# Performance work log

Measured on AMD Instinct MI355X. Metric: run time of the kernel, lower is better.

The kernel has to match this reference:

```python
import jax, jax.numpy as jnp
import numpy as np

T, B, S, L = 256, 128, 256, 2
H, E, V = 512, 512, 32000


def setup_inputs() -> dict:
    key = jax.random.key(0)
    ks = jax.random.split(key, 17)
    n = lambda k, shape, s=0.05: jax.random.normal(k, shape, dtype=jnp.float32) * s
    tokens = jax.random.randint(ks[0], (T, B), 0, V)
    emb = n(ks[1], (V, E)).at[0].set(0.0)  # padding_idx=0 row zeroed
    return {
        "tokens": tokens,
        "h0": n(ks[2], (L, B, H)),
        "c0": n(ks[3], (L, B, H)),
        "context": n(ks[4], (S, B, H)),
        "init_output": n(ks[5], (B, H)),
        "emb": emb,
        "W_ih0": n(ks[6], (4 * H, E + H)),
        "b_ih0": n(ks[7], (4 * H,)),
        "W_hh0": n(ks[8], (4 * H, H)),
        "b_hh0": n(ks[9], (4 * H,)),
        "W_ih1": n(ks[10], (4 * H, H)),
        "b_ih1": n(ks[11], (4 * H,)),
        "W_hh1": n(ks[12], (4 * H, H)),
        "b_hh1": n(ks[13], (4 * H,)),
        "W_in": n(ks[14], (H, H)),
        "W_out": n(ks[15], (H, 2 * H)),
    }


def _lstm_cell(x, h, c, Wi, bi, Wh, bh):
    # torch LSTMCell: gates ordered i, f, g, o
    g = x @ Wi.T + bi + h @ Wh.T + bh
    i, f, gg, o = jnp.split(g, 4, axis=-1)
    c2 = jax.nn.sigmoid(f) * c + jax.nn.sigmoid(i) * jnp.tanh(gg)
    h2 = jax.nn.sigmoid(o) * jnp.tanh(c2)
    return h2, c2


def reference(tokens, h0, c0, context, init_output, emb,
              W_ih0, b_ih0, W_hh0, b_hh0, W_ih1, b_ih1, W_hh1, b_hh1,
              W_in, W_out):
    emb_seq = emb[tokens]                      # [T, B, E]
    ctx = jnp.transpose(context, (1, 0, 2))    # [B, S, H] (context.transpose(0,1))

    def step(carry, e_t):
        h, c, out = carry                      # h,c: [L,B,H]; out: [B,H]
        x = jnp.concatenate([e_t, out], axis=1)  # input feed
        h0_, c0_ = _lstm_cell(x, h[0], c[0], W_ih0, b_ih0, W_hh0, b_hh0)
        h1_, c1_ = _lstm_cell(h0_, h[1], c[1], W_ih1, b_ih1, W_hh1, b_hh1)
        rnn_out = h1_                          # dropout is identity at p=0 / eval
        # GlobalAttention (Luong general): score = ctx @ (W_in h)
        q = rnn_out @ W_in.T                   # [B, H]
        scores = jnp.einsum('bsh,bh->bs', ctx, q)
        a = jax.nn.softmax(scores, axis=-1)    # [B, S]
        wc = jnp.einsum('bs,bsh->bh', a, ctx)  # weighted context
        attn_out = jnp.tanh(jnp.concatenate([wc, rnn_out], axis=1) @ W_out.T)
        new_h = jnp.stack([h0_, h1_])
        new_c = jnp.stack([c0_, c1_])
        return (new_h, new_c, attn_out), (attn_out, a)

    (hF, cF, _), (outputs, attns) = jax.lax.scan(step, (h0, c0, init_output), emb_seq)
    return outputs, hF, cF, attns[-1]
```

## Files before the change

kernel.cpp:

```cpp
#include <hip/hip_runtime.h>
#include <hip/hip_bf16.h>
#include <math.h>

#define TT 256
#define BB 128
#define SS 256
#define HH 512
#define EE 512
#define NBLK 128
#define NTHR 512
#define BH (BB * HH)

typedef __attribute__((ext_vector_type(4))) float f32x4;
typedef __attribute__((ext_vector_type(8))) short s16x8;
typedef unsigned long long u64;

__device__ __forceinline__ float b2f(short v) {
    union { unsigned u; float f; } c;
    c.u = ((unsigned)(unsigned short)v) << 16;
    return c.f;
}
__device__ __forceinline__ short f2b(float f) {
    union { float f; unsigned u; } c; c.f = f;
    unsigned u = c.u;
    unsigned r = (u + 0x7fffu + ((u >> 16) & 1u)) >> 16;
    return (short)r;
}
__device__ __forceinline__ float sigm(float x) { return 1.f / (1.f + __expf(-x)); }

__device__ __forceinline__ u64 aldq(const void* p) {
    return __hip_atomic_load((const u64*)p, __ATOMIC_RELAXED, __HIP_MEMORY_SCOPE_AGENT);
}
__device__ __forceinline__ void ast2(short* p, short v) {
    __hip_atomic_store(p, v, __ATOMIC_RELAXED, __HIP_MEMORY_SCOPE_AGENT);
}
__device__ __forceinline__ s16x8 ald16(const void* p) {
    s16x8 r;
    asm volatile("global_load_dwordx4 %0, %1, off sc0 sc1" : "=v"(r) : "v"(p) : "memory");
    return r;
}

__device__ __forceinline__ void lbar() {
    asm volatile("s_waitcnt lgkmcnt(0)" ::: "memory");
    __builtin_amdgcn_s_barrier();
}


__global__ void k_pack2(const float* __restrict__ Wa, int ka, const float* __restrict__ Wb, int kb,
                        short* __restrict__ dst, int n) {
    const int K = ka + kb;
    for (int i = blockIdx.x * blockDim.x + threadIdx.x; i < n; i += gridDim.x * blockDim.x) {
        int g = i / K, k = i - g * K;
        float v = (k < ka) ? Wa[(size_t)g * ka + k] : Wb[(size_t)g * kb + (k - ka)];
        dst[i] = f2b(v);
    }
}

__global__ void k_bias(const float* __restrict__ a, const float* __restrict__ b, float* __restrict__ o,
                       const float* __restrict__ a2, const float* __restrict__ b2, float* __restrict__ o2) {
    int i = blockIdx.x * blockDim.x + threadIdx.x;
    if (i < 2048) { o[i] = a[i] + b[i]; o2[i] = a2[i] + b2[i]; }
}

__global__ void k_emb(const int* __restrict__ tok, const float* __restrict__ emb, short* __restrict__ Ebf) {
    const int n = TT * BB * EE;
    for (int i = blockIdx.x * blockDim.x + threadIdx.x; i < n; i += gridDim.x * blockDim.x) {
        int tb = i >> 9, k = i & 511;
        int t = tok[tb];
        Ebf[i] = f2b(emb[(size_t)t * EE + k]);
    }
}

__global__ __launch_bounds__(512) void k_cvt8(const float* __restrict__ ctx, const short* __restrict__ Wb,
                                              int wstride, int transpose, unsigned char* __restrict__ out8) {
    const int tid = threadIdx.x, w = tid >> 6, l = tid & 63;
    const int m0 = blockIdx.y * 128, n0 = blockIdx.x * 64;
    const int kc8 = (l >> 4) * 8;
    const int m = m0 + w * 16 + (l & 15);
    const int b = m >> 8, s = m & 255;
    const float* arow = ctx + ((size_t)s * BB + b) * HH + kc8;
    f32x4 acc[4];
    const f32x4 zero = {0.f, 0.f, 0.f, 0.f};
#pragma unroll
    for (int j = 0; j < 4; ++j) acc[j] = zero;
#pragma unroll
    for (int kc = 0; kc < 16; ++kc) {
        const int k0 = kc * 32;
        float4 x0 = *reinterpret_cast<const float4*>(arow + k0);
        float4 x1 = *reinterpret_cast<const float4*>(arow + k0 + 4);
        s16x8 afr;
        afr[0] = f2b(x0.x); afr[1] = f2b(x0.y); afr[2] = f2b(x0.z); afr[3] = f2b(x0.w);
        afr[4] = f2b(x1.x); afr[5] = f2b(x1.y); afr[6] = f2b(x1.z); afr[7] = f2b(x1.w);
#pragma unroll
        for (int j = 0; j < 4; ++j) {
            s16x8 bfr = *reinterpret_cast<const s16x8*>(Wb + (size_t)(n0 + j * 16 + (l & 15)) * wstride + k0 + kc8);
            acc[j] = __builtin_amdgcn_mfma_f32_16x16x32_bf16(afr, bfr, acc[j], 0, 0, 0);
        }
    }
#pragma unroll
    for (int j = 0; j < 4; ++j)
#pragma unroll
        for (int r = 0; r < 4; ++r) {
            const int mm = m0 + w * 16 + (l >> 4) * 4 + r;
            const int nn = n0 + j * 16 + (l & 15);
            unsigned char v8 = (unsigned char)(__builtin_amdgcn_cvt_pk_fp8_f32(acc[j][r], 0.f, 0, false) & 0xff);
            if (transpose) {
                const int bb = mm >> 8, ss = mm & 255;
                out8[((size_t)bb * HH + nn) * SS + ss] = v8;
            } else {
                out8[(size_t)mm * HH + nn] = v8;
            }
        }
}

__global__ void k_state(const float* __restrict__ h0in, const float* __restrict__ iout,
                        short* __restrict__ h0x, short* __restrict__ h1x, short* __restrict__ outx) {
    int i = blockIdx.x * blockDim.x + threadIdx.x;
    if (i < BH) {
        h0x[i] = f2b(h0in[i]);
        h1x[i] = f2b(h0in[BH + i]);
        outx[i] = f2b(iout[i]);
    }
}


struct P {
    const short* Ebf;
    const float* c0in;
    const unsigned char* ctxW8;
    const unsigned char* ctxO8T;
    const short* Woutb;
    const short* W0cat;
    const short* W1cat;
    const float* bias0;
    const float* bias1;
    short* h0x;
    short* h1x;
    short* outx;
    float* dout;
    unsigned* flags;
};

#define MFMA16(a, b, c) __builtin_amdgcn_mfma_f32_16x16x32_bf16((a), (b), (c), 0, 0, 0)
#define MFMA8(a, b, c) __builtin_amdgcn_mfma_f32_16x16x32_fp8_fp8((a), (b), (c), 0, 0, 0)

__device__ __forceinline__ s16x8 ldsfrag(const short* base, int stride, int row, int col8) {
    return *reinterpret_cast<const s16x8*>(base + row * stride + ((col8 ^ (row & 7)) << 3));
}

__device__ __forceinline__ void issue8(const short* __restrict__ src, int tid, int khalf, s16x8* q) {
#pragma unroll
    for (int c = 0; c < 8; ++c) {
        const int chunk = c * 512 + tid;
        const int row = chunk >> 5, col8 = chunk & 31;
        q[c] = ald16(src + row * HH + khalf * 256 + col8 * 8);
    }
}
template <int N>
__device__ __forceinline__ void write8n(short* __restrict__ stg, int tid, const s16x8* q) {
    asm volatile("s_waitcnt vmcnt(%0)" ::"i"(N) : "memory");
#pragma unroll
    for (int c = 0; c < 8; ++c) {
        const int chunk = c * 512 + tid;
        const int row = chunk >> 5, col8 = chunk & 31;
        *reinterpret_cast<s16x8*>(stg + row * 256 + ((col8 ^ (row & 7)) << 3)) = q[c];
    }
}

__device__ __forceinline__ f32x4 seg8(const short* stgp, const short* Ws, int wstride, int wbase,
                                      int mrow, int wrow, int kq, f32x4 acc) {
#pragma unroll
    for (int seg = 0; seg < 8; ++seg)
        acc = MFMA16(ldsfrag(stgp, 256, mrow, seg * 4 + kq),
                     ldsfrag(Ws, wstride, wrow, wbase + seg * 4 + kq), acc);
    return acc;
}

__device__ __forceinline__ void gbar(unsigned* flags, unsigned target) {
    asm volatile("s_waitcnt vmcnt(0)" ::: "memory");
    __syncthreads();
    if (threadIdx.x == 0)
        __hip_atomic_store(&flags[blockIdx.x * 16], target, __ATOMIC_RELAXED, __HIP_MEMORY_SCOPE_AGENT);
    if (threadIdx.x < NBLK) {
        while (__hip_atomic_load(&flags[threadIdx.x * 16], __ATOMIC_RELAXED, __HIP_MEMORY_SCOPE_AGENT) < target)
            __builtin_amdgcn_s_sleep(8);
    }
    __syncthreads();
}

__global__ void __launch_bounds__(NTHR, 1) coop_k(P p) {
    extern __shared__ __align__(16) char smem[];
    short* W0s = (short*)smem;
    short* W1s = W0s + 16 * 1536;
    short* stg = W1s + 16 * 1024;
    float* smallf = (float*)(stg + 128 * 256);
    float* bias0s = smallf;
    float* bias1s = smallf + 16;
    float* red = smallf + 32;
    float* scv = smallf + 48;
    float* aU = smallf + 304;
    short* h1b = (short*)(smallf + 560);
    unsigned* h18u = (unsigned*)(smallf + 816);
    unsigned* a32 = (unsigned*)(smallf + 944);

    const int tid = threadIdx.x;
    const int blk = blockIdx.x;
    const int l = tid & 63;
    const int w = tid >> 6;
    const int lrow = l & 15;
    const int mrow = w * 16 + lrow;
    const int kq = l >> 4;
    const size_t OFF_HF = (size_t)TT * BH;
    const size_t OFF_CF = OFF_HF + 2 * (size_t)BH;
    const size_t OFF_AT = OFF_CF + 2 * (size_t)BH;
    const f32x4 fz = {0.f, 0.f, 0.f, 0.f};

    for (int idx = tid; idx < 16 * 192; idx += NTHR) {
        int row = idx / 192, col8 = idx % 192;
        int g = (row & 3) * 512 + blk * 4 + (row >> 2);
        *reinterpret_cast<s16x8*>(W0s + row * 1536 + ((col8 ^ (row & 7)) << 3)) =
            *reinterpret_cast<const s16x8*>(p.W0cat + (size_t)g * 1536 + col8 * 8);
    }
    for (int idx = tid; idx < 16 * 128; idx += NTHR) {
        int row = idx / 128, col8 = idx % 128;
        int g = (row & 3) * 512 + blk * 4 + (row >> 2);
        *reinterpret_cast<s16x8*>(W1s + row * 1024 + ((col8 ^ (row & 7)) << 3)) =
            *reinterpret_cast<const s16x8*>(p.W1cat + (size_t)g * 1024 + col8 * 8);
    }
    if (tid < 16) {
        int g = (tid & 3) * 512 + blk * 4 + (tid >> 2);
        bias0s[tid] = p.bias0[g];
        bias1s[tid] = p.bias1[g];
    }
    __syncthreads();

    const int bA = tid >> 2;
    const int jA = blk * 4 + (tid & 3);
    float c0reg = p.c0in[bA * HH + jA];
    float c1reg = p.c0in[BH + bA * HH + jA];
    unsigned ep = 0;
    s16x8 qa[8], qb[8], qc[8], qd[8];

    for (int t = 0; t < TT; ++t) {
        const size_t pB = (size_t)(t & 1) * BH;
        const size_t pN = (size_t)((t & 1) ^ 1) * BH;

        {
            issue8(p.outx + pB, tid, 0, qa);
            issue8(p.outx + pB, tid, 1, qb);
            f32x4 aE = fz, aO = fz, aH = fz;
            {
                const short* erow = p.Ebf + ((size_t)t * BB + mrow) * EE + kq * 8;
#pragma unroll
                for (int seg = 0; seg < 16; ++seg) {
                    s16x8 afr = *reinterpret_cast<const s16x8*>(erow + seg * 32);
                    aE = MFMA16(afr, ldsfrag(W0s, 1536, lrow, seg * 4 + kq), aE);
                }
            }
            write8n<8>(stg, tid, qa);
            issue8(p.h0x + pB, tid, 0, qc);
            lbar();
            aO = seg8(stg, W0s, 1536, 64, mrow, lrow, kq, aO);
            lbar();
            write8n<8>(stg, tid, qb);
            issue8(p.h0x + pB, tid, 1, qd);
            lbar();
            aO = seg8(stg, W0s, 1536, 96, mrow, lrow, kq, aO);
            lbar();
            write8n<8>(stg, tid, qc);
            lbar();
            aH = seg8(stg, W0s, 1536, 128, mrow, lrow, kq, aH);
            lbar();
            write8n<0>(stg, tid, qd);
            lbar();
            aH = seg8(stg, W0s, 1536, 160, mrow, lrow, kq, aH);

            f32x4 acc = aE + aO + aH;
            lbar();
            float* scr = (float*)stg + w * 272;
#pragma unroll
            for (int r = 0; r < 4; ++r) scr[lrow * 17 + kq * 4 + r] = acc[r];
            const int bloc = l >> 2;
            const int n0 = (l & 3) * 4;
            float gi = scr[(n0 + 0) * 17 + bloc] + bias0s[n0 + 0];
            float gf = scr[(n0 + 1) * 17 + bloc] + bias0s[n0 + 1];
            float gg = scr[(n0 + 2) * 17 + bloc] + bias0s[n0 + 2];
            float go = scr[(n0 + 3) * 17 + bloc] + bias0s[n0 + 3];
            float cn = sigm(gf) * c0reg + sigm(gi) * tanhf(gg);
            float hn = sigm(go) * tanhf(cn);
            c0reg = cn;
            ast2(&p.h0x[pN + bA * HH + jA], f2b(hn));
            if (t == TT - 1) {
                p.dout[OFF_HF + bA * HH + jA] = hn;
                p.dout[OFF_CF + bA * HH + jA] = cn;
            }
        }
        gbar(p.flags, ++ep);

        {
            issue8(p.h0x + pN, tid, 0, qa);
            issue8(p.h0x + pN, tid, 1, qb);
            f32x4 b0 = fz, b1 = fz;
            write8n<8>(stg, tid, qa);
            issue8(p.h1x + pB, tid, 0, qc);
            lbar();
            b0 = seg8(stg, W1s, 1024, 0, mrow, lrow, kq, b0);
            lbar();
            write8n<8>(stg, tid, qb);
            issue8(p.h1x + pB, tid, 1, qd);
            lbar();
            b0 = seg8(stg, W1s, 1024, 32, mrow, lrow, kq, b0);
            lbar();
            write8n<8>(stg, tid, qc);
            lbar();
            b1 = seg8(stg, W1s, 1024, 64, mrow, lrow, kq, b1);
            lbar();
            write8n<0>(stg, tid, qd);
            lbar();
            b1 = seg8(stg, W1s, 1024, 96, mrow, lrow, kq, b1);

            f32x4 acc = b0 + b1;
            lbar();
            float* scr = (float*)stg + w * 272;
#pragma unroll
            for (int r = 0; r < 4; ++r) scr[lrow * 17 + kq * 4 + r] = acc[r];
            const int bloc = l >> 2;
            const int n0 = (l & 3) * 4;
            float gi = scr[(n0 + 0) * 17 + bloc] + bias1s[n0 + 0];
            float gf = scr[(n0 + 1) * 17 + bloc] + bias1s[n0 + 1];
            float gg = scr[(n0 + 2) * 17 + bloc] + bias1s[n0 + 2];
            float go = scr[(n0 + 3) * 17 + bloc] + bias1s[n0 + 3];
            float cn = sigm(gf) * c1reg + sigm(gi) * tanhf(gg);
            float hn = sigm(go) * tanhf(cn);
            c1reg = cn;
            ast2(&p.h1x[pN + bA * HH + jA], f2b(hn));
            if (t == TT - 1) {
                p.dout[OFF_HF + BH + bA * HH + jA] = hn;
                p.dout[OFF_CF + BH + bA * HH + jA] = cn;
            }
        }
        gbar(p.flags, ++ep);

        {
            float* pFh = (float*)stg;
            if (tid < 128) {
                union { u64 v; short s[4]; } c;
                c.v = aldq(p.h1x + pN + blk * HH + tid * 4);
#pragma unroll
                for (int j = 0; j < 4; ++j) h1b[tid * 4 + j] = c.s[j];
                float f0 = b2f(c.s[0]), f1 = b2f(c.s[1]), f2 = b2f(c.s[2]), f3 = b2f(c.s[3]);
                unsigned lo = __builtin_amdgcn_cvt_pk_fp8_f32(f0, f1, 0, false) & 0xffffu;
                unsigned hi = __builtin_amdgcn_cvt_pk_fp8_f32(f2, f3, 0, false) & 0xffffu;
                h18u[tid] = lo | (hi << 16);
            }
            lbar();
            {
                const unsigned char* cwb = p.ctxW8 + (size_t)blk * SS * HH;
                const u64* h18q = (const u64*)h18u;
#pragma unroll
                for (int i = 0; i < 2; ++i) {
                    const int s0 = (w * 2 + i) * 16;
                    f32x4 acc = fz;
#pragma unroll
                    for (int kc = 0; kc < 16; ++kc) {
                        const int k0 = kc * 32;
                        long long av = (long long)h18q[(k0 >> 3) + kq];
                        long long bv = *reinterpret_cast<const long long*>(cwb + (size_t)(s0 + lrow) * HH + k0 + kq * 8);
                        acc = MFMA8(av, bv, acc);
                    }
                    if (l < 16) scv[s0 + l] = acc[0];
                }
            }
            lbar();
            float sc = -1e30f, e = 0.f;
            if (tid < 256) sc = scv[tid];
            float mx = sc;
#pragma unroll
            for (int off = 32; off; off >>= 1) mx = fmaxf(mx, __shfl_xor(mx, off));
            if (l == 0 && tid < 256) red[w] = mx;
            lbar();
            const float M = fmaxf(fmaxf(red[0], red[1]), fmaxf(red[2], red[3]));
            if (tid < 256) { e = __expf(sc - M); aU[tid] = e; }
            float se = e;
#pragma unroll
            for (int off = 32; off; off >>= 1) se += __shfl_xor(se, off);
            if (l == 0 && tid < 256) red[8 + w] = se;
            lbar();
            const float inv = 1.f / (red[8] + red[9] + red[10] + red[11]);
            if (t == TT - 1 && tid < 256) p.dout[OFF_AT + blk * SS + tid] = aU[tid] * inv;
            if (tid < 64) {
                unsigned lo = __builtin_amdgcn_cvt_pk_fp8_f32(aU[tid * 4], aU[tid * 4 + 1], 0, false) & 0xffffu;
                unsigned hi = __builtin_amdgcn_cvt_pk_fp8_f32(aU[tid * 4 + 2], aU[tid * 4 + 3], 0, false) & 0xffffu;
                a32[tid] = lo | (hi << 16);
            }
            f32x4 gacc[4];
#pragma unroll
            for (int i = 0; i < 4; ++i) {
                const int j0 = (w * 4 + i) * 16;
                f32x4 acc = fz;
#pragma unroll
                for (int kc = 0; kc < 16; ++kc) {
                    const int k0 = kc * 32;
                    s16x8 av = *reinterpret_cast<const s16x8*>(h1b + k0 + kq * 8);
                    s16x8 bv = *reinterpret_cast<const s16x8*>(p.Woutb + (size_t)(j0 + lrow) * 1024 + 512 + k0 + kq * 8);
                    acc = MFMA16(av, bv, acc);
                }
                gacc[i] = acc;
            }
            lbar();
            {
                const unsigned char* cob = p.ctxO8T + (size_t)blk * HH * SS;
                const u64* a8q = (const u64*)a32;
#pragma unroll
                for (int i = 0; i < 4; ++i) {
                    const int h0 = (w * 4 + i) * 16;
                    f32x4 acc = fz;
#pragma unroll
                    for (int kc = 0; kc < 8; ++kc) {
                        const int k0 = kc * 32;
                        long long av = (long long)a8q[(k0 >> 3) + kq];
                        long long bv = *reinterpret_cast<const long long*>(cob + (size_t)(h0 + lrow) * SS + k0 + kq * 8);
                        acc = MFMA8(av, bv, acc);
                    }
                    if (l < 16) pFh[h0 + l] = acc[0];
                }
            }
            lbar();
#pragma unroll
            for (int i = 0; i < 4; ++i) {
                if (l < 16) {
                    const int j = (w * 4 + i) * 16 + l;
                    float tv = tanhf(pFh[j] * inv + gacc[i][0]);
                    __builtin_nontemporal_store(tv, &p.dout[(size_t)t * BH + blk * HH + j]);
                    ast2(&p.outx[pN + blk * HH + j], f2b(tv));
                }
            }
        }
        gbar(p.flags, ++ep);
    }
}


extern "C" void kernel_launch(void* const* d_in, const int* in_sizes, int n_in,
                              void* d_out, int out_size, void* d_ws, size_t ws_size,
                              hipStream_t stream) {
    const int* tokens = (const int*)d_in[0];
    const float* h0in = (const float*)d_in[1];
    const float* c0in = (const float*)d_in[2];
    const float* ctx = (const float*)d_in[3];
    const float* iout = (const float*)d_in[4];
    const float* emb = (const float*)d_in[5];
    const float* Wih0 = (const float*)d_in[6];
    const float* bih0 = (const float*)d_in[7];
    const float* Whh0 = (const float*)d_in[8];
    const float* bhh0 = (const float*)d_in[9];
    const float* Wih1 = (const float*)d_in[10];
    const float* bih1 = (const float*)d_in[11];
    const float* Whh1 = (const float*)d_in[12];
    const float* bhh1 = (const float*)d_in[13];
    const float* Win = (const float*)d_in[14];
    const float* Wout = (const float*)d_in[15];
    float* dout = (float*)d_out;

    char* pw = (char*)d_ws;
    auto take = [&](size_t bytes) { char* r = pw; pw += (bytes + 255) & ~(size_t)255; return r; };
    short* W0cat = (short*)take((size_t)2048 * 1536 * 2);
    short* W1cat = (short*)take((size_t)2048 * 1024 * 2);
    short* Winb  = (short*)take((size_t)512 * 512 * 2);
    short* Woutb = (short*)take((size_t)512 * 1024 * 2);
    float* bias0 = (float*)take(2048 * 4);
    float* bias1 = (float*)take(2048 * 4);
    short* Ebf   = (short*)take((size_t)TT * BB * EE * 2);
    unsigned char* ctxW8 = (unsigned char*)take((size_t)BB * SS * HH);
    unsigned char* ctxO8T = (unsigned char*)take((size_t)BB * SS * HH);
    short* h0x   = (short*)take((size_t)2 * BH * 2);
    short* h1x   = (short*)take((size_t)2 * BH * 2);
    short* outx  = (short*)take((size_t)2 * BH * 2);
    unsigned* flags = (unsigned*)take(NBLK * 64);

    k_pack2<<<2048, 256, 0, stream>>>(Wih0, 1024, Whh0, 512, W0cat, 2048 * 1536);
    k_pack2<<<2048, 256, 0, stream>>>(Wih1, 512, Whh1, 512, W1cat, 2048 * 1024);
    k_pack2<<<1024, 256, 0, stream>>>(Win, 512, Win, 0, Winb, 512 * 512);
    k_pack2<<<1024, 256, 0, stream>>>(Wout, 1024, Wout, 0, Woutb, 512 * 1024);
    k_bias<<<8, 256, 0, stream>>>(bih0, bhh0, bias0, bih1, bhh1, bias1);
    k_emb<<<4096, 256, 0, stream>>>(tokens, emb, Ebf);
    k_state<<<256, 256, 0, stream>>>(h0in, iout, h0x, h1x, outx);
    k_cvt8<<<dim3(8, 256), 512, 0, stream>>>(ctx, Winb, 512, 0, ctxW8);
    k_cvt8<<<dim3(8, 256), 512, 0, stream>>>(ctx, Woutb, 1024, 1, ctxO8T);
    (void)hipMemsetAsync(flags, 0, NBLK * 64, stream);

    const unsigned smem_bytes = (16 * 1536 + 16 * 1024 + 128 * 256) * 2 + 1008 * 4;
    (void)hipFuncSetAttribute((const void*)coop_k, hipFuncAttributeMaxDynamicSharedMemorySize, (int)smem_bytes);

    P prm;
    prm.Ebf = Ebf; prm.c0in = c0in;
    prm.ctxW8 = ctxW8; prm.ctxO8T = ctxO8T; prm.Woutb = Woutb;
    prm.W0cat = W0cat; prm.W1cat = W1cat;
    prm.bias0 = bias0; prm.bias1 = bias1;
    prm.h0x = h0x; prm.h1x = h1x; prm.outx = outx;
    prm.dout = dout; prm.flags = flags;
    void* args[] = {&prm};
    (void)hipLaunchCooperativeKernel((void*)coop_k, dim3(NBLK), dim3(NTHR), args, smem_bytes, stream);
}
```

Baseline: 12.93 ms.

## Keep raw fp8 context and compute attention projections per step instead of precomputed products

Replaces the two precomputed context-times-weight fp8 tensors (ctx·W_in^T and transposed ctx·W_out) with one plain fp8 copy of the context. Each step now computes q = W_in·h1 with bf16 MFMA, stages 128-row context tiles in padded LDS for the score MFMAs, builds the weighted context with scalar fp8-decode FMAs, and applies W_out to the concatenated [wc, h1] vector. This halves per-step context traffic and removes the two large preprocessing GEMMs. In exchange it adds per-step W_in and full W_out matvecs, extra LDS staging and barriers, and a scalar reduction loop in place of an MFMA.

```diff
diff --git a/kernel.cpp b/kernel.cpp
--- a/kernel.cpp
+++ b/kernel.cpp
@@ -12,6 +12,7 @@
 #define BH (BB * HH)
 
 typedef __attribute__((ext_vector_type(4))) float f32x4;
+typedef __attribute__((ext_vector_type(2))) float f32x2;
 typedef __attribute__((ext_vector_type(8))) short s16x8;
 typedef unsigned long long u64;
 
@@ -27,6 +28,10 @@
     return (short)r;
 }
 __device__ __forceinline__ float sigm(float x) { return 1.f / (1.f + __expf(-x)); }
+
+__device__ __forceinline__ unsigned short f2fp8x2(float x, float y) {
+    return (unsigned short)(__builtin_amdgcn_cvt_pk_fp8_f32(x, y, 0, false) & 0xffff);
+}
 
 __device__ __forceinline__ u64 aldq(const void* p) {
     return __hip_atomic_load((const u64*)p, __ATOMIC_RELAXED, __HIP_MEMORY_SCOPE_AGENT);
@@ -71,46 +76,15 @@
     }
 }
 
-__global__ __launch_bounds__(512) void k_cvt8(const float* __restrict__ ctx, const short* __restrict__ Wb,
-                                              int wstride, int transpose, unsigned char* __restrict__ out8) {
-    const int tid = threadIdx.x, w = tid >> 6, l = tid & 63;
-    const int m0 = blockIdx.y * 128, n0 = blockIdx.x * 64;
-    const int kc8 = (l >> 4) * 8;
-    const int m = m0 + w * 16 + (l & 15);
-    const int b = m >> 8, s = m & 255;
-    const float* arow = ctx + ((size_t)s * BB + b) * HH + kc8;
-    f32x4 acc[4];
-    const f32x4 zero = {0.f, 0.f, 0.f, 0.f};
-#pragma unroll
-    for (int j = 0; j < 4; ++j) acc[j] = zero;
-#pragma unroll
-    for (int kc = 0; kc < 16; ++kc) {
-        const int k0 = kc * 32;
-        float4 x0 = *reinterpret_cast<const float4*>(arow + k0);
-        float4 x1 = *reinterpret_cast<const float4*>(arow + k0 + 4);
-        s16x8 afr;
-        afr[0] = f2b(x0.x); afr[1] = f2b(x0.y); afr[2] = f2b(x0.z); afr[3] = f2b(x0.w);
-        afr[4] = f2b(x1.x); afr[5] = f2b(x1.y); afr[6] = f2b(x1.z); afr[7] = f2b(x1.w);
-#pragma unroll
-        for (int j = 0; j < 4; ++j) {
-            s16x8 bfr = *reinterpret_cast<const s16x8*>(Wb + (size_t)(n0 + j * 16 + (l & 15)) * wstride + k0 + kc8);
-            acc[j] = __builtin_amdgcn_mfma_f32_16x16x32_bf16(afr, bfr, acc[j], 0, 0, 0);
-        }
-    }
-#pragma unroll
-    for (int j = 0; j < 4; ++j)
-#pragma unroll
-        for (int r = 0; r < 4; ++r) {
-            const int mm = m0 + w * 16 + (l >> 4) * 4 + r;
-            const int nn = n0 + j * 16 + (l & 15);
-            unsigned char v8 = (unsigned char)(__builtin_amdgcn_cvt_pk_fp8_f32(acc[j][r], 0.f, 0, false) & 0xff);
-            if (transpose) {
-                const int bb = mm >> 8, ss = mm & 255;
-                out8[((size_t)bb * HH + nn) * SS + ss] = v8;
-            } else {
-                out8[(size_t)mm * HH + nn] = v8;
-            }
-        }
+__global__ void k_ctx8(const float* __restrict__ ctx, unsigned char* __restrict__ c8) {
+    const int n2 = BB * SS * (HH / 2);
+    for (int i = blockIdx.x * blockDim.x + threadIdx.x; i < n2; i += gridDim.x * blockDim.x) {
+        int h2 = i & 255, rest = i >> 8;
+        int s = rest & 255, b = rest >> 8;
+        int h = h2 * 2;
+        const float* src = ctx + ((size_t)s * BB + b) * HH + h;
+        *reinterpret_cast<unsigned short*>(c8 + ((size_t)b * SS + s) * HH + h) = f2fp8x2(src[0], src[1]);
+    }
 }
 
 __global__ void k_state(const float* __restrict__ h0in, const float* __restrict__ iout,
@@ -127,8 +101,8 @@
 struct P {
     const short* Ebf;
     const float* c0in;
-    const unsigned char* ctxW8;
-    const unsigned char* ctxO8T;
+    const unsigned char* ctxb8;
+    const short* Winb;
     const short* Woutb;
     const short* W0cat;
     const short* W1cat;
@@ -144,6 +118,8 @@
 #define MFMA16(a, b, c) __builtin_amdgcn_mfma_f32_16x16x32_bf16((a), (b), (c), 0, 0, 0)
 #define MFMA8(a, b, c) __builtin_amdgcn_mfma_f32_16x16x32_fp8_fp8((a), (b), (c), 0, 0, 0)
 
+#define CSTRIDE 536
+
 __device__ __forceinline__ s16x8 ldsfrag(const short* base, int stride, int row, int col8) {
     return *reinterpret_cast<const s16x8*>(base + row * stride + ((col8 ^ (row & 7)) << 3));
 }
@@ -193,15 +169,14 @@
     short* W0s = (short*)smem;
     short* W1s = W0s + 16 * 1536;
     short* stg = W1s + 16 * 1024;
-    float* smallf = (float*)(stg + 128 * 256);
-    float* bias0s = smallf;
-    float* bias1s = smallf + 16;
-    float* red = smallf + 32;
-    float* scv = smallf + 48;
-    float* aU = smallf + 304;
-    short* h1b = (short*)(smallf + 560);
-    unsigned* h18u = (unsigned*)(smallf + 816);
-    unsigned* a32 = (unsigned*)(smallf + 944);
+    char* smallc = (char*)stg + 128 * CSTRIDE;
+    float* bias0s = (float*)smallc;
+    float* bias1s = bias0s + 16;
+    float* red = bias1s + 16;
+    float* scv = red + 16;
+    float* aU = scv + 256;
+    short* catb = (short*)(aU + 256);
+    unsigned char* q8b = (unsigned char*)(catb + 1024);
 
     const int tid = threadIdx.x;
     const int blk = blockIdx.x;
@@ -342,33 +317,57 @@
         gbar(p.flags, ++ep);
 
         {
-            float* pFh = (float*)stg;
+            unsigned char* ctile = (unsigned char*)stg;
+            float* pF = (float*)stg;
+            const unsigned char* cgb = p.ctxb8 + (size_t)blk * SS * HH;
             if (tid < 128) {
-                union { u64 v; short s[4]; } c;
-                c.v = aldq(p.h1x + pN + blk * HH + tid * 4);
-#pragma unroll
-                for (int j = 0; j < 4; ++j) h1b[tid * 4 + j] = c.s[j];
-                float f0 = b2f(c.s[0]), f1 = b2f(c.s[1]), f2 = b2f(c.s[2]), f3 = b2f(c.s[3]);
-                unsigned lo = __builtin_amdgcn_cvt_pk_fp8_f32(f0, f1, 0, false) & 0xffffu;
-                unsigned hi = __builtin_amdgcn_cvt_pk_fp8_f32(f2, f3, 0, false) & 0xffffu;
-                h18u[tid] = lo | (hi << 16);
-            }
-            lbar();
-            {
-                const unsigned char* cwb = p.ctxW8 + (size_t)blk * SS * HH;
-                const u64* h18q = (const u64*)h18u;
-#pragma unroll
-                for (int i = 0; i < 2; ++i) {
-                    const int s0 = (w * 2 + i) * 16;
+                u64 v = aldq(p.h1x + pN + blk * HH + tid * 4);
+                *reinterpret_cast<u64*>(catb + 512 + tid * 4) = v;
+            }
+            lbar();
+#pragma unroll
+            for (int i = 0; i < 4; ++i) {
+                const int j0 = (w * 4 + i) * 16;
+                f32x4 acc = fz;
+#pragma unroll
+                for (int kc = 0; kc < 16; ++kc) {
+                    const int k0 = kc * 32;
+                    s16x8 av = *reinterpret_cast<const s16x8*>(catb + 512 + k0 + kq * 8);
+                    s16x8 bv = *reinterpret_cast<const s16x8*>(p.Winb + (size_t)(j0 + lrow) * 512 + k0 + kq * 8);
+                    acc = MFMA16(av, bv, acc);
+                }
+                if (l < 16)
+                    q8b[j0 + l] = (unsigned char)(__builtin_amdgcn_cvt_pk_fp8_f32(acc[0], 0.f, 0, false) & 0xff);
+            }
+#pragma unroll
+            for (int half = 0; half < 2; ++half) {
+                lbar();
+                {
+                    const int srow = tid >> 2, seg = tid & 3;
+                    const unsigned char* gsrc = cgb + (size_t)(half * 128 + srow) * HH + seg * 128;
+                    char* drow = (char*)ctile + (size_t)srow * CSTRIDE + seg * 128;
+#pragma unroll
+                    for (int j = 0; j < 8; ++j) {
+                        union { float4 f; u64 q[2]; } cc;
+                        cc.f = *reinterpret_cast<const float4*>(gsrc + j * 16);
+                        u64* d = reinterpret_cast<u64*>(drow + j * 16);
+                        d[0] = cc.q[0];
+                        d[1] = cc.q[1];
+                    }
+                }
+                lbar();
+                {
+                    const u64* q8q = (const u64*)q8b;
                     f32x4 acc = fz;
 #pragma unroll
                     for (int kc = 0; kc < 16; ++kc) {
                         const int k0 = kc * 32;
-                        long long av = (long long)h18q[(k0 >> 3) + kq];
-                        long long bv = *reinterpret_cast<const long long*>(cwb + (size_t)(s0 + lrow) * HH + k0 + kq * 8);
+                        long long av = (long long)q8q[(k0 >> 3) + kq];
+                        long long bv = (long long)*reinterpret_cast<const u64*>(
+                            (const char*)ctile + (size_t)(w * 16 + lrow) * CSTRIDE + k0 + kq * 8);
                         acc = MFMA8(av, bv, acc);
                     }
-                    if (l < 16) scv[s0 + l] = acc[0];
+                    if (l < 16) scv[half * 128 + w * 16 + l] = acc[0];
                 }
             }
             lbar();
@@ -388,49 +387,45 @@
             lbar();
             const float inv = 1.f / (red[8] + red[9] + red[10] + red[11]);
             if (t == TT - 1 && tid < 256) p.dout[OFF_AT + blk * SS + tid] = aU[tid] * inv;
-            if (tid < 64) {
-                unsigned lo = __builtin_amdgcn_cvt_pk_fp8_f32(aU[tid * 4], aU[tid * 4 + 1], 0, false) & 0xffffu;
-                unsigned hi = __builtin_amdgcn_cvt_pk_fp8_f32(aU[tid * 4 + 2], aU[tid * 4 + 3], 0, false) & 0xffffu;
-                a32[tid] = lo | (hi << 16);
-            }
-            f32x4 gacc[4];
+            {
+                const int hd = tid & 127;
+                const int sg = tid >> 7;
+                float pv0 = 0.f, pv1 = 0.f, pv2 = 0.f, pv3 = 0.f;
+#pragma unroll 8
+                for (int s = sg * 64; s < sg * 64 + 64; ++s) {
+                    const float av = aU[s];
+                    unsigned dv = *reinterpret_cast<const unsigned*>(cgb + (size_t)s * HH + hd * 4);
+                    f32x2 lo = __builtin_amdgcn_cvt_pk_f32_fp8(dv, false);
+                    f32x2 hi = __builtin_amdgcn_cvt_pk_f32_fp8(dv, true);
+                    pv0 += av * lo[0];
+                    pv1 += av * lo[1];
+                    pv2 += av * hi[0];
+                    pv3 += av * hi[1];
+                }
+                lbar();
+                float4 vv = {pv0, pv1, pv2, pv3};
+                *reinterpret_cast<float4*>(pF + sg * 512 + hd * 4) = vv;
+            }
+            lbar();
+            {
+                float wc = (pF[tid] + pF[512 + tid] + pF[1024 + tid] + pF[1536 + tid]) * inv;
+                catb[tid] = f2b(wc);
+            }
+            lbar();
 #pragma unroll
             for (int i = 0; i < 4; ++i) {
                 const int j0 = (w * 4 + i) * 16;
                 f32x4 acc = fz;
 #pragma unroll
-                for (int kc = 0; kc < 16; ++kc) {
+                for (int kc = 0; kc < 32; ++kc) {
                     const int k0 = kc * 32;
-                    s16x8 av = *reinterpret_cast<const s16x8*>(h1b + k0 + kq * 8);
-                    s16x8 bv = *reinterpret_cast<const s16x8*>(p.Woutb + (size_t)(j0 + lrow) * 1024 + 512 + k0 + kq * 8);
+                    s16x8 av = *reinterpret_cast<const s16x8*>(catb + k0 + kq * 8);
+                    s16x8 bv = *reinterpret_cast<const s16x8*>(p.Woutb + (size_t)(j0 + lrow) * 1024 + k0 + kq * 8);
                     acc = MFMA16(av, bv, acc);
                 }
-                gacc[i] = acc;
-            }
-            lbar();
-            {
-                const unsigned char* cob = p.ctxO8T + (size_t)blk * HH * SS;
-                const u64* a8q = (const u64*)a32;
-#pragma unroll
-                for (int i = 0; i < 4; ++i) {
-                    const int h0 = (w * 4 + i) * 16;
-                    f32x4 acc = fz;
-#pragma unroll
-                    for (int kc = 0; kc < 8; ++kc) {
-                        const int k0 = kc * 32;
-                        long long av = (long long)a8q[(k0 >> 3) + kq];
-                        long long bv = *reinterpret_cast<const long long*>(cob + (size_t)(h0 + lrow) * SS + k0 + kq * 8);
-                        acc = MFMA8(av, bv, acc);
-                    }
-                    if (l < 16) pFh[h0 + l] = acc[0];
-                }
-            }
-            lbar();
-#pragma unroll
-            for (int i = 0; i < 4; ++i) {
                 if (l < 16) {
-                    const int j = (w * 4 + i) * 16 + l;
-                    float tv = tanhf(pFh[j] * inv + gacc[i][0]);
+                    const int j = j0 + l;
+                    float tv = tanhf(acc[0]);
                     __builtin_nontemporal_store(tv, &p.dout[(size_t)t * BH + blk * HH + j]);
                     ast2(&p.outx[pN + blk * HH + j], f2b(tv));
                 }
@@ -471,8 +466,7 @@
     float* bias0 = (float*)take(2048 * 4);
     float* bias1 = (float*)take(2048 * 4);
     short* Ebf   = (short*)take((size_t)TT * BB * EE * 2);
-    unsigned char* ctxW8 = (unsigned char*)take((size_t)BB * SS * HH);
-    unsigned char* ctxO8T = (unsigned char*)take((size_t)BB * SS * HH);
+    unsigned char* ctxb8 = (unsigned char*)take((size_t)BB * SS * HH);
     short* h0x   = (short*)take((size_t)2 * BH * 2);
     short* h1x   = (short*)take((size_t)2 * BH * 2);
     short* outx  = (short*)take((size_t)2 * BH * 2);
@@ -484,17 +478,16 @@
     k_pack2<<<1024, 256, 0, stream>>>(Wout, 1024, Wout, 0, Woutb, 512 * 1024);
     k_bias<<<8, 256, 0, stream>>>(bih0, bhh0, bias0, bih1, bhh1, bias1);
     k_emb<<<4096, 256, 0, stream>>>(tokens, emb, Ebf);
+    k_ctx8<<<4096, 256, 0, stream>>>(ctx, ctxb8);
     k_state<<<256, 256, 0, stream>>>(h0in, iout, h0x, h1x, outx);
-    k_cvt8<<<dim3(8, 256), 512, 0, stream>>>(ctx, Winb, 512, 0, ctxW8);
-    k_cvt8<<<dim3(8, 256), 512, 0, stream>>>(ctx, Woutb, 1024, 1, ctxO8T);
     (void)hipMemsetAsync(flags, 0, NBLK * 64, stream);
 
-    const unsigned smem_bytes = (16 * 1536 + 16 * 1024 + 128 * 256) * 2 + 1008 * 4;
+    const unsigned smem_bytes = (16 * 1536 + 16 * 1024) * 2 + 128 * CSTRIDE + (16 + 16 + 16 + 256 + 256) * 4 + 1024 * 2 + 512;
     (void)hipFuncSetAttribute((const void*)coop_k, hipFuncAttributeMaxDynamicSharedMemorySize, (int)smem_bytes);
 
     P prm;
     prm.Ebf = Ebf; prm.c0in = c0in;
-    prm.ctxW8 = ctxW8; prm.ctxO8T = ctxO8T; prm.Woutb = Woutb;
+    prm.ctxb8 = ctxb8; prm.Winb = Winb; prm.Woutb = Woutb;
     prm.W0cat = W0cat; prm.W1cat = W1cat;
     prm.bias0 = bias0; prm.bias1 = bias1;
     prm.h0x = h0x; prm.h1x = h1x; prm.outx = outx;
```

New measurement: 20.02 ms. 54.9% more time.

## Write h states to per-timestep buffers, use cached loads, fuse embedding gather

Applied to the files above, without the earlier changes.

Hidden states h0/h1 now go to a fresh slot for every timestep instead of a ping-pong pair. No cache line is ever rewritten, so readers can use normal cached loads rather than sc0/sc1 system-coherent loads. The separate embedding gather/convert kernel is also removed; the persistent kernel reads fp32 embedding rows by token and converts them to bf16 inline. This trades a larger workspace and extra in-loop conversion for less pre-pass traffic and cheaper state loads. It relies on the never-rewritten addresses leaving no stale L2 or cache lines across CUs.

```diff
diff --git a/kernel.cpp b/kernel.cpp
--- a/kernel.cpp
+++ b/kernel.cpp
@@ -28,6 +28,10 @@
 }
 __device__ __forceinline__ float sigm(float x) { return 1.f / (1.f + __expf(-x)); }
 
+__device__ __forceinline__ unsigned short f2fp8x2(float x, float y) {
+    return (unsigned short)(__builtin_amdgcn_cvt_pk_fp8_f32(x, y, 0, false) & 0xffff);
+}
+
 __device__ __forceinline__ u64 aldq(const void* p) {
     return __hip_atomic_load((const u64*)p, __ATOMIC_RELAXED, __HIP_MEMORY_SCOPE_AGENT);
 }
@@ -37,6 +41,11 @@
 __device__ __forceinline__ s16x8 ald16(const void* p) {
     s16x8 r;
     asm volatile("global_load_dwordx4 %0, %1, off sc0 sc1" : "=v"(r) : "v"(p) : "memory");
+    return r;
+}
+__device__ __forceinline__ s16x8 ald16c(const void* p) {
+    s16x8 r;
+    asm volatile("global_load_dwordx4 %0, %1, off" : "=v"(r) : "v"(p) : "memory");
     return r;
 }
 
@@ -60,15 +69,6 @@
                        const float* __restrict__ a2, const float* __restrict__ b2, float* __restrict__ o2) {
     int i = blockIdx.x * blockDim.x + threadIdx.x;
     if (i < 2048) { o[i] = a[i] + b[i]; o2[i] = a2[i] + b2[i]; }
-}
-
-__global__ void k_emb(const int* __restrict__ tok, const float* __restrict__ emb, short* __restrict__ Ebf) {
-    const int n = TT * BB * EE;
-    for (int i = blockIdx.x * blockDim.x + threadIdx.x; i < n; i += gridDim.x * blockDim.x) {
-        int tb = i >> 9, k = i & 511;
-        int t = tok[tb];
-        Ebf[i] = f2b(emb[(size_t)t * EE + k]);
-    }
 }
 
 __global__ __launch_bounds__(512) void k_cvt8(const float* __restrict__ ctx, const short* __restrict__ Wb,
@@ -114,18 +114,19 @@
 }
 
 __global__ void k_state(const float* __restrict__ h0in, const float* __restrict__ iout,
-                        short* __restrict__ h0x, short* __restrict__ h1x, short* __restrict__ outx) {
+                        short* __restrict__ h0r, short* __restrict__ h1r, short* __restrict__ outx) {
     int i = blockIdx.x * blockDim.x + threadIdx.x;
     if (i < BH) {
-        h0x[i] = f2b(h0in[i]);
-        h1x[i] = f2b(h0in[BH + i]);
+        h0r[i] = f2b(h0in[i]);
+        h1r[i] = f2b(h0in[BH + i]);
         outx[i] = f2b(iout[i]);
     }
 }
 
 
 struct P {
-    const short* Ebf;
+    const int* tokens;
+    const float* emb;
     const float* c0in;
     const unsigned char* ctxW8;
     const unsigned char* ctxO8T;
@@ -134,8 +135,8 @@
     const short* W1cat;
     const float* bias0;
     const float* bias1;
-    short* h0x;
-    short* h1x;
+    short* h0r;
+    short* h1r;
     short* outx;
     float* dout;
     unsigned* flags;
@@ -148,12 +149,14 @@
     return *reinterpret_cast<const s16x8*>(base + row * stride + ((col8 ^ (row & 7)) << 3));
 }
 
+template <bool CACHED>
 __device__ __forceinline__ void issue8(const short* __restrict__ src, int tid, int khalf, s16x8* q) {
 #pragma unroll
     for (int c = 0; c < 8; ++c) {
         const int chunk = c * 512 + tid;
         const int row = chunk >> 5, col8 = chunk & 31;
-        q[c] = ald16(src + row * HH + khalf * 256 + col8 * 8);
+        const short* a = src + row * HH + khalf * 256 + col8 * 8;
+        q[c] = CACHED ? ald16c(a) : ald16(a);
     }
 }
 template <int N>
@@ -244,26 +247,35 @@
     for (int t = 0; t < TT; ++t) {
         const size_t pB = (size_t)(t & 1) * BH;
         const size_t pN = (size_t)((t & 1) ^ 1) * BH;
+        const short* h0old = p.h0r + (size_t)t * BH;
+        short* h0new = p.h0r + (size_t)(t + 1) * BH;
+        const short* h1old = p.h1r + (size_t)t * BH;
+        short* h1new = p.h1r + (size_t)(t + 1) * BH;
 
         {
-            issue8(p.outx + pB, tid, 0, qa);
-            issue8(p.outx + pB, tid, 1, qb);
+            issue8<false>(p.outx + pB, tid, 0, qa);
+            issue8<false>(p.outx + pB, tid, 1, qb);
             f32x4 aE = fz, aO = fz, aH = fz;
             {
-                const short* erow = p.Ebf + ((size_t)t * BB + mrow) * EE + kq * 8;
+                const int tok = p.tokens[t * BB + mrow];
+                const float* erow = p.emb + (size_t)tok * EE + kq * 8;
 #pragma unroll
                 for (int seg = 0; seg < 16; ++seg) {
-                    s16x8 afr = *reinterpret_cast<const s16x8*>(erow + seg * 32);
+                    float4 x0 = *reinterpret_cast<const float4*>(erow + seg * 32);
+                    float4 x1 = *reinterpret_cast<const float4*>(erow + seg * 32 + 4);
+                    s16x8 afr;
+                    afr[0] = f2b(x0.x); afr[1] = f2b(x0.y); afr[2] = f2b(x0.z); afr[3] = f2b(x0.w);
+                    afr[4] = f2b(x1.x); afr[5] = f2b(x1.y); afr[6] = f2b(x1.z); afr[7] = f2b(x1.w);
                     aE = MFMA16(afr, ldsfrag(W0s, 1536, lrow, seg * 4 + kq), aE);
                 }
             }
             write8n<8>(stg, tid, qa);
-            issue8(p.h0x + pB, tid, 0, qc);
+            issue8<true>(h0old, tid, 0, qc);
             lbar();
             aO = seg8(stg, W0s, 1536, 64, mrow, lrow, kq, aO);
             lbar();
             write8n<8>(stg, tid, qb);
-            issue8(p.h0x + pB, tid, 1, qd);
+            issue8<true>(h0old, tid, 1, qd);
             lbar();
             aO = seg8(stg, W0s, 1536, 96, mrow, lrow, kq, aO);
             lbar();
@@ -289,7 +301,7 @@
             float cn = sigm(gf) * c0reg + sigm(gi) * tanhf(gg);
             float hn = sigm(go) * tanhf(cn);
             c0reg = cn;
-            ast2(&p.h0x[pN + bA * HH + jA], f2b(hn));
+            ast2(&h0new[bA * HH + jA], f2b(hn));
             if (t == TT - 1) {
                 p.dout[OFF_HF + bA * HH + jA] = hn;
                 p.dout[OFF_CF + bA * HH + jA] = cn;
@@ -298,16 +310,16 @@
         gbar(p.flags, ++ep);
 
         {
-            issue8(p.h0x + pN, tid, 0, qa);
-            issue8(p.h0x + pN, tid, 1, qb);
+            issue8<true>(h0new, tid, 0, qa);
+            issue8<true>(h0new, tid, 1, qb);
             f32x4 b0 = fz, b1 = fz;
             write8n<8>(stg, tid, qa);
-            issue8(p.h1x + pB, tid, 0, qc);
+            issue8<true>(h1old, tid, 0, qc);
             lbar();
             b0 = seg8(stg, W1s, 1024, 0, mrow, lrow, kq, b0);
             lbar();
             write8n<8>(stg, tid, qb);
-            issue8(p.h1x + pB, tid, 1, qd);
+            issue8<true>(h1old, tid, 1, qd);
             lbar();
             b0 = seg8(stg, W1s, 1024, 32, mrow, lrow, kq, b0);
             lbar();
@@ -333,7 +345,7 @@
             float cn = sigm(gf) * c1reg + sigm(gi) * tanhf(gg);
             float hn = sigm(go) * tanhf(cn);
             c1reg = cn;
-            ast2(&p.h1x[pN + bA * HH + jA], f2b(hn));
+            ast2(&h1new[bA * HH + jA], f2b(hn));
             if (t == TT - 1) {
                 p.dout[OFF_HF + BH + bA * HH + jA] = hn;
                 p.dout[OFF_CF + BH + bA * HH + jA] = cn;
@@ -345,7 +357,7 @@
             float* pFh = (float*)stg;
             if (tid < 128) {
                 union { u64 v; short s[4]; } c;
-                c.v = aldq(p.h1x + pN + blk * HH + tid * 4);
+                c.v = *reinterpret_cast<const u64*>(h1new + blk * HH + tid * 4);
 #pragma unroll
                 for (int j = 0; j < 4; ++j) h1b[tid * 4 + j] = c.s[j];
                 float f0 = b2f(c.s[0]), f1 = b2f(c.s[1]), f2 = b2f(c.s[2]), f3 = b2f(c.s[3]);
@@ -470,11 +482,10 @@
     short* Woutb = (short*)take((size_t)512 * 1024 * 2);
     float* bias0 = (float*)take(2048 * 4);
     float* bias1 = (float*)take(2048 * 4);
-    short* Ebf   = (short*)take((size_t)TT * BB * EE * 2);
     unsigned char* ctxW8 = (unsigned char*)take((size_t)BB * SS * HH);
     unsigned char* ctxO8T = (unsigned char*)take((size_t)BB * SS * HH);
-    short* h0x   = (short*)take((size_t)2 * BH * 2);
-    short* h1x   = (short*)take((size_t)2 * BH * 2);
+    short* h0r   = (short*)take((size_t)(TT + 1) * BH * 2);
+    short* h1r   = (short*)take((size_t)(TT + 1) * BH * 2);
     short* outx  = (short*)take((size_t)2 * BH * 2);
     unsigned* flags = (unsigned*)take(NBLK * 64);
 
@@ -483,8 +494,7 @@
     k_pack2<<<1024, 256, 0, stream>>>(Win, 512, Win, 0, Winb, 512 * 512);
     k_pack2<<<1024, 256, 0, stream>>>(Wout, 1024, Wout, 0, Woutb, 512 * 1024);
     k_bias<<<8, 256, 0, stream>>>(bih0, bhh0, bias0, bih1, bhh1, bias1);
-    k_emb<<<4096, 256, 0, stream>>>(tokens, emb, Ebf);
-    k_state<<<256, 256, 0, stream>>>(h0in, iout, h0x, h1x, outx);
+    k_state<<<256, 256, 0, stream>>>(h0in, iout, h0r, h1r, outx);
     k_cvt8<<<dim3(8, 256), 512, 0, stream>>>(ctx, Winb, 512, 0, ctxW8);
     k_cvt8<<<dim3(8, 256), 512, 0, stream>>>(ctx, Woutb, 1024, 1, ctxO8T);
     (void)hipMemsetAsync(flags, 0, NBLK * 64, stream);
@@ -493,11 +503,11 @@
     (void)hipFuncSetAttribute((const void*)coop_k, hipFuncAttributeMaxDynamicSharedMemorySize, (int)smem_bytes);
 
     P prm;
-    prm.Ebf = Ebf; prm.c0in = c0in;
+    prm.tokens = tokens; prm.emb = emb; prm.c0in = c0in;
     prm.ctxW8 = ctxW8; prm.ctxO8T = ctxO8T; prm.Woutb = Woutb;
     prm.W0cat = W0cat; prm.W1cat = W1cat;
     prm.bias0 = bias0; prm.bias1 = bias1;
-    prm.h0x = h0x; prm.h1x = h1x; prm.outx = outx;
+    prm.h0r = h0r; prm.h1r = h1r; prm.outx = outx;
     prm.dout = dout; prm.flags = flags;
     void* args[] = {&prm};
     (void)hipLaunchCooperativeKernel((void*)coop_k, dim3(NBLK), dim3(NTHR), args, smem_bytes, stream);
```

After: 13.91 ms. 7.7% more time.
